# Kernel optimization log

Hardware: AMD Instinct MI355X
Metric: run time of the kernel (lower is better)

## Reference

```python
import jax, jax.numpy as jnp
from jax import lax
import numpy as np

N_QUBITS = 4
N_LAYERS = 2


def _apply_gate(state, M, w):
    # state: [B, 2,2,2,2]; M: [2,2] shared or [B,2,2] batched; acts on wire w
    s = jnp.moveaxis(state, w + 1, 1)
    if M.ndim == 3:
        s = jnp.einsum('bij,bj...->bi...', M, s)
    else:
        s = jnp.einsum('ij,bj...->bi...', M, s)
    return jnp.moveaxis(s, 1, w + 1)


def _apply_cnot(state, c, t):
    # c < t always (chain CNOTs). Move control axis to 1; target axis (t+1) unchanged.
    s = jnp.moveaxis(state, c + 1, 1)
    s0 = s[:, 0]
    s1 = jnp.flip(s[:, 1], axis=t)  # target axis after dropping axis1 is t+1-1 = t
    s = jnp.stack([s0, s1], axis=1)
    return jnp.moveaxis(s, 1, c + 1)


def _quantum_head(q_input, qparams):
    # q_input: [B, n_qubits] rotation angles; qparams: [n_layers, n_qubits, 3]
    B = q_input.shape[0]
    state = jnp.zeros((B, 2 ** N_QUBITS), jnp.complex64).at[:, 0].set(1.0)
    state = state.reshape((B,) + (2,) * N_QUBITS)
    # RY feature map (batched matrices)
    for i in range(N_QUBITS):
        th = q_input[:, i]
        c, s = jnp.cos(th / 2), jnp.sin(th / 2)
        M = jnp.stack([jnp.stack([c, -s], -1), jnp.stack([s, c], -1)], -2)  # [B,2,2]
        state = _apply_gate(state, M.astype(jnp.complex64), i)
    # variational layers
    for layer in range(N_LAYERS):
        for i in range(N_QUBITS):
            phi = qparams[layer, i, 0]
            th = qparams[layer, i, 1]
            om = qparams[layer, i, 2]
            c, s = jnp.cos(th / 2), jnp.sin(th / 2)
            hs, hd = 0.5 * (phi + om), 0.5 * (phi - om)
            M = jnp.stack([
                jnp.stack([jnp.exp(-1j * hs) * c, -jnp.exp(1j * hd) * s]),
                jnp.stack([jnp.exp(-1j * hd) * s, jnp.exp(1j * hs) * c]),
            ])  # [2,2] shared across batch (Rot = RZ(om) RY(th) RZ(phi))
            state = _apply_gate(state, M.astype(jnp.complex64), i)
        for i in range(N_QUBITS - 1):
            state = _apply_cnot(state, i, i + 1)
    # <Z_0> = P(q0=0) - P(q0=1)
    probs = state.real ** 2 + state.imag ** 2
    probs = probs.reshape(B, 2, -1)
    return probs[:, 0].sum(-1) - probs[:, 1].sum(-1)


def _maxpool21(x):
    return lax.reduce_window(x, -np.inf, lax.max, (1, 1, 2, 2), (1, 1, 1, 1), 'VALID')


def setup_inputs() -> dict:
    key = jax.random.key(0)
    ks = jax.random.split(key, 8)
    r = lambda k, s, sc: jax.random.normal(k, s, jnp.float32) * sc
    return {
        'inputs': jax.random.normal(ks[0], (128, 3, 250, 250), jnp.float32),
        'conv1_w': r(ks[1], (6, 3, 5, 5), 0.1),
        'conv1_b': jnp.zeros((6,), jnp.float32),
        'conv2_w': r(ks[2], (15, 6, 3, 3), 0.1),
        'conv2_b': jnp.zeros((15,), jnp.float32),
        'fc1_w': r(ks[3], (120, 55815), 0.004),
        'fc1_b': jnp.zeros((120,), jnp.float32),
        'fc2_w': r(ks[4], (84, 120), 0.09),
        'fc2_b': jnp.zeros((84,), jnp.float32),
        'fc3_w': r(ks[5], (1, 84), 0.1),
        'fc3_b': jnp.zeros((1,), jnp.float32),
        'qparams': jax.random.normal(ks[6], (N_LAYERS, N_QUBITS, 3), jnp.float32),
    }


def reference(inputs, conv1_w, conv1_b, conv2_w, conv2_b, fc1_w, fc1_b,
              fc2_w, fc2_b, fc3_w, fc3_b, qparams):
    dn = ('NCHW', 'OIHW', 'NCHW')
    x = lax.conv_general_dilated(inputs, conv1_w, (2, 2), [(1, 1), (1, 1)],
                                 dimension_numbers=dn) + conv1_b[None, :, None, None]
    x = _maxpool21(jax.nn.relu(x))          # [B,6,123,123]
    x = lax.conv_general_dilated(x, conv2_w, (2, 2), [(1, 1), (1, 1)],
                                 dimension_numbers=dn) + conv2_b[None, :, None, None]
    x = _maxpool21(jax.nn.relu(x))          # [B,15,61,61]
    x = x.reshape(x.shape[0], -1)           # [B,55815]
    x = jax.nn.relu(x @ fc1_w.T + fc1_b)
    x = jax.nn.relu(x @ fc2_w.T + fc2_b)
    x = (x @ fc3_w.T + fc3_b)[:, 0]         # [B]
    q_input = jnp.repeat(x[:, None], N_QUBITS, axis=1)
    q_out = _quantum_head(q_input, qparams)  # [B]
    probs = 0.5 * (q_out + 1.0)
    return jnp.stack([probs, 1.0 - probs], axis=-1)
```

## Files before the change

### kernel.cpp

```cpp
#include <hip/hip_runtime.h>

#define SPLITK 256
#define FC1_K 55815

__global__ __launch_bounds__(256) void conv1f_k(const float* __restrict__ in,
                                                const float* __restrict__ w,
                                                const float* __restrict__ bias,
                                                float* __restrict__ out) {
    __shared__ float sbuf[4608];
    const int tc = blockIdx.x, tr = blockIdx.y, b = blockIdx.z;
    const int pr0 = tr * 31, pc0 = tc * 31;
    const int tid = threadIdx.x;
    const int i = tid >> 4, j = tid & 15;
    const float* inb = in + (size_t)b * 187500;
    const int ir0 = 2 * pr0 - 1, ic0 = 2 * pc0 - 1;

    float acc[6][2][2];
    #pragma unroll
    for (int o = 0; o < 6; ++o) {
        float bv = bias[o];
        acc[o][0][0] = bv; acc[o][0][1] = bv; acc[o][1][0] = bv; acc[o][1][1] = bv;
    }

    float stg[18];
    auto load_ch = [&](int c) {
        const float* cp = inb + c * 62500;
        int y = tid / 68;
        int x = tid - y * 68;
        #pragma unroll
        for (int it = 0; it < 18; ++it) {
            int gr = ir0 + y, gc = ic0 + x;
            float v = 0.0f;
            if ((unsigned)gr < 250u && (unsigned)gc < 250u)
                v = cp[gr * 250 + gc];
            stg[it] = v;
            x += 52; y += 3;
            if (x >= 68) { x -= 68; ++y; }
        }
    };
    auto write_ch = [&]() {
        #pragma unroll
        for (int it = 0; it < 18; ++it) sbuf[tid + it * 256] = stg[it];
    };
    auto compute_ch = [&](int c) {
        #pragma unroll
        for (int wr = 0; wr < 7; ++wr) {
            const float* rp = &sbuf[(4 * i + wr) * 68 + 4 * j];
            float row[7];
            float4 v4 = *(const float4*)rp;
            float2 v2 = *(const float2*)(rp + 4);
            row[0] = v4.x; row[1] = v4.y; row[2] = v4.z; row[3] = v4.w;
            row[4] = v2.x; row[5] = v2.y; row[6] = rp[6];
            #pragma unroll
            for (int o = 0; o < 6; ++o) {
                #pragma unroll
                for (int kw = 0; kw < 5; ++kw) {
                    if (wr <= 4) {
                        float wv = w[o * 75 + c * 25 + wr * 5 + kw];
                        acc[o][0][0] = fmaf(row[kw], wv, acc[o][0][0]);
                        acc[o][0][1] = fmaf(row[kw + 2], wv, acc[o][0][1]);
                    }
                    if (wr >= 2) {
                        float wv = w[o * 75 + c * 25 + (wr - 2) * 5 + kw];
                        acc[o][1][0] = fmaf(row[kw], wv, acc[o][1][0]);
                        acc[o][1][1] = fmaf(row[kw + 2], wv, acc[o][1][1]);
                    }
                }
            }
        }
    };

    load_ch(0); write_ch();
    __syncthreads();
    load_ch(1); compute_ch(0);
    __syncthreads();
    write_ch();
    __syncthreads();
    load_ch(2); compute_ch(1);
    __syncthreads();
    write_ch();
    __syncthreads();
    compute_ch(2);
    __syncthreads();

    const int gr0 = pr0 + 2 * i, gc0 = pc0 + 2 * j;
    const bool r1in = (2 * i + 1 < 31) && (gr0 + 1 < 123);
    const bool c1in = (2 * j + 1 < 31) && (gc0 + 1 < 123);
    const bool r0in = gr0 < 123, c0in = gc0 < 123;
    #pragma unroll
    for (int g = 0; g < 2; ++g) {
        #pragma unroll
        for (int oo = 0; oo < 3; ++oo)
            #pragma unroll
            for (int di = 0; di < 2; ++di)
                #pragma unroll
                for (int dj = 0; dj < 2; ++dj)
                    sbuf[(oo * 32 + 2 * i + di) * 33 + (2 * j + dj)] =
                        fmaxf(acc[g * 3 + oo][di][dj], 0.0f);
        __syncthreads();
        #pragma unroll
        for (int oo = 0; oo < 3; ++oo) {
            int o = g * 3 + oo;
            const float* p0 = &sbuf[(oo * 32 + 2 * i) * 33 + 2 * j];
            float c00 = p0[0],  c01 = p0[1],  c02 = p0[2];
            float c10 = p0[33], c11 = p0[34], c12 = p0[35];
            float c20 = p0[66], c21 = p0[67], c22 = p0[68];
            float* orow = out + ((size_t)(b * 6 + o) * 123 + gr0) * 123 + gc0;
            if (r0in && c0in) orow[0]   = fmaxf(fmaxf(c00, c01), fmaxf(c10, c11));
            if (r0in && c1in) orow[1]   = fmaxf(fmaxf(c01, c02), fmaxf(c11, c12));
            if (r1in && c0in) orow[123] = fmaxf(fmaxf(c10, c11), fmaxf(c20, c21));
            if (r1in && c1in) orow[124] = fmaxf(fmaxf(c11, c12), fmaxf(c21, c22));
        }
        __syncthreads();
    }
}

__global__ __launch_bounds__(256) void conv2f_k(const float* __restrict__ in,
                                                const float* __restrict__ w,
                                                const float* __restrict__ bias,
                                                float* __restrict__ out) {
    __shared__ float smem[2000];
    const int tc = blockIdx.x, tr = blockIdx.y, b = blockIdx.z;
    const int pr0 = tr * 15, pc0 = tc * 15;
    const int tid = threadIdx.x;
    const int wv = tid >> 6, lane = tid & 63;
    const int ti = tid >> 4, tj = tid & 15;
    const int tl = ti & 3;
    float* wreg = smem + wv * 320;
    float* halo = smem + 1280;
    const float* inb = in + (size_t)b * 6 * 15129;
    const int irw = 2 * pr0 - 1 + 8 * wv;
    const int ic0 = 2 * pc0 - 1;
    const bool safe = (tr >= 1 && tr <= 3) && (tc >= 1 && tc <= 3);

    int off[5];
    unsigned msk = 0u;
    {
        int y = (lane >= 34) ? 1 : 0;
        int x = lane - 34 * y;
        #pragma unroll
        for (int it = 0; it < 5; ++it) {
            int gr = irw + y, gc = ic0 + x;
            bool valid = ((unsigned)gr < 123u) && ((unsigned)gc < 123u);
            off[it] = valid ? (gr * 123 + gc) : 0;
            msk |= (valid ? 1u : 0u) << it;
            x += 30; ++y;
            if (x >= 34) { x -= 34; ++y; }
        }
    }

    float acc[15];
    #pragma unroll
    for (int o = 0; o < 15; ++o) acc[o] = bias[o];

    for (int c = 0; c < 6; ++c) {
        const float* cp = inb + c * 15129;
        if (safe) {
            #pragma unroll
            for (int it = 0; it < 5; ++it) wreg[lane + it * 64] = cp[off[it]];
        } else {
            #pragma unroll
            for (int it = 0; it < 5; ++it) {
                float v = 0.0f;
                if ((msk >> it) & 1u) v = cp[off[it]];
                wreg[lane + it * 64] = v;
            }
        }
        #pragma unroll
        for (int kh = 0; kh < 3; ++kh) {
            const float* r = &wreg[(2 * tl + kh) * 34 + 2 * tj];
            float a0 = r[0], a1 = r[1], a2 = r[2];
            #pragma unroll
            for (int o = 0; o < 15; ++o) {
                const float* wr_ = &w[o * 54 + c * 9 + kh * 3];
                acc[o] = fmaf(a0, wr_[0], acc[o]);
                acc[o] = fmaf(a1, wr_[1], acc[o]);
                acc[o] = fmaf(a2, wr_[2], acc[o]);
            }
        }
    }

    if (tl == 0 && wv > 0) {
        #pragma unroll
        for (int o = 0; o < 15; ++o)
            halo[(wv - 1) * 240 + o * 16 + tj] = acc[o];
    }
    __syncthreads();

    const int gr = pr0 + ti, gc = pc0 + tj;
    const bool valid = (ti < 15) && (tj < 15) && (gr < 61) && (gc < 61);
    const bool lastrow = (tl == 3);
    const int hb = (wv < 2 ? wv : 2) * 240;
    #pragma unroll
    for (int o = 0; o < 15; ++o) {
        float c00 = acc[o];
        float c01 = __shfl(acc[o], lane + 1);
        float s10 = __shfl(acc[o], lane + 16);
        float s11 = __shfl(acc[o], lane + 17);
        float h10 = halo[hb + o * 16 + tj];
        float h11 = halo[hb + o * 16 + (tj + 1 > 15 ? 15 : tj + 1)];
        float c10 = lastrow ? h10 : s10;
        float c11 = lastrow ? h11 : s11;
        float m = fmaxf(fmaxf(fmaxf(c00, c01), fmaxf(c10, c11)), 0.0f);
        if (valid) out[((size_t)(b * 15 + o) * 61 + gr) * 61 + gc] = m;
    }
}

__global__ __launch_bounds__(256) void fc1_k(const float* __restrict__ X,
                                             const float* __restrict__ W,
                                             float* __restrict__ P) {
    __shared__ float Xs[2][16][132];
    __shared__ float Ws[2][16][66];
    const int K = FC1_K;
    const int chunk = (K + SPLITK - 1) / SPLITK;
    const int s = blockIdx.x, nh = blockIdx.y;
    const int n0 = nh * 60;
    int ks = s * chunk;
    int ke = min(ks + chunk, K);
    int tid = threadIdx.x;
    const int tx = tid & 15, ty = tid >> 4;
    const int kk_ = tid & 15, r0_ = tid >> 4;
    float acc[8][4];
    #pragma unroll
    for (int ii = 0; ii < 8; ++ii)
        #pragma unroll
        for (int jj = 0; jj < 4; ++jj) acc[ii][jj] = 0.0f;

    float nx[8], nw[4];
    auto ld = [&](int k0n) {
        int krem = ke - k0n;
        int k = k0n + kk_;
        bool kv = kk_ < krem;
        #pragma unroll
        for (int it = 0; it < 8; ++it) {
            int r = r0_ + it * 16;
            nx[it] = kv ? X[(size_t)r * K + k] : 0.0f;
        }
        #pragma unroll
        for (int it = 0; it < 4; ++it) {
            int r = r0_ + it * 16;
            nw[it] = (kv && r < 60) ? W[(size_t)(n0 + r) * K + k] : 0.0f;
        }
    };
    auto st = [&](int buf) {
        #pragma unroll
        for (int it = 0; it < 8; ++it) Xs[buf][kk_][r0_ + it * 16] = nx[it];
        #pragma unroll
        for (int it = 0; it < 4; ++it) Ws[buf][kk_][r0_ + it * 16] = nw[it];
    };

    if (ks < ke) { ld(ks); st(0); }
    int cur = 0;
    for (int k0 = ks; k0 < ke; k0 += 16) {
        __syncthreads();
        bool hn = (k0 + 16) < ke;
        if (hn) ld(k0 + 16);
        #pragma unroll
        for (int kk = 0; kk < 16; ++kk) {
            float4 xa = *(const float4*)&Xs[cur][kk][ty * 8];
            float4 xb = *(const float4*)&Xs[cur][kk][ty * 8 + 4];
            float4 wb = *(const float4*)&Ws[cur][kk][tx * 4];
            float av[8] = {xa.x, xa.y, xa.z, xa.w, xb.x, xb.y, xb.z, xb.w};
            float bv[4] = {wb.x, wb.y, wb.z, wb.w};
            #pragma unroll
            for (int ii = 0; ii < 8; ++ii)
                #pragma unroll
                for (int jj = 0; jj < 4; ++jj)
                    acc[ii][jj] = fmaf(av[ii], bv[jj], acc[ii][jj]);
        }
        if (hn) st(cur ^ 1);
        cur ^= 1;
    }
    float* Pp = P + (size_t)s * 15360;
    #pragma unroll
    for (int ii = 0; ii < 8; ++ii) {
        int m = ty * 8 + ii;
        #pragma unroll
        for (int jj = 0; jj < 4; ++jj) {
            int nn = tx * 4 + jj;
            if (nn < 60) Pp[m * 120 + n0 + nn] = acc[ii][jj];
        }
    }
}

__global__ __launch_bounds__(256) void tail_k(const float* __restrict__ P,
                                              const float* __restrict__ f1b,
                                              const float* __restrict__ f2w,
                                              const float* __restrict__ f2b,
                                              const float* __restrict__ f3w,
                                              const float* __restrict__ f3b,
                                              const float* __restrict__ qp,
                                              float* __restrict__ out) {
    __shared__ float red[2][120];
    __shared__ float x1[120];
    __shared__ float x2[84];
    int b = blockIdx.x, tid = threadIdx.x;
    if (tid < 240) {
        int part = tid / 120;
        int n = tid - part * 120;
        const float* p = P + (size_t)b * 120 + n;
        float acc = 0.0f;
        #pragma unroll 8
        for (int s = part; s < SPLITK; s += 2)
            acc += p[(size_t)s * 15360];
        red[part][n] = acc;
    }
    __syncthreads();
    if (tid < 120)
        x1[tid] = fmaxf(red[0][tid] + red[1][tid] + f1b[tid], 0.0f);
    __syncthreads();
    if (tid < 84) {
        float acc = f2b[tid];
        const float* wr = f2w + tid * 120;
        #pragma unroll 4
        for (int n = 0; n < 120; ++n) acc = fmaf(x1[n], wr[n], acc);
        x2[tid] = fmaxf(acc, 0.0f);
    }
    __syncthreads();
    if (tid == 0) {
        float x = f3b[0];
        for (int m = 0; m < 84; ++m) x = fmaf(x2[m], f3w[m], x);
        float sr[16], si[16];
        #pragma unroll
        for (int i = 0; i < 16; ++i) { sr[i] = 0.0f; si[i] = 0.0f; }
        sr[0] = 1.0f;
        float c0 = cosf(0.5f * x), s0 = sinf(0.5f * x);
        #pragma unroll
        for (int w = 0; w < 4; ++w) {
            int mask = 8 >> w;
            #pragma unroll
            for (int idx = 0; idx < 16; ++idx) {
                if (idx & mask) continue;
                int i1 = idx | mask;
                float a0r = sr[idx], a0i = si[idx], a1r = sr[i1], a1i = si[i1];
                sr[idx] = c0 * a0r - s0 * a1r;  si[idx] = c0 * a0i - s0 * a1i;
                sr[i1]  = s0 * a0r + c0 * a1r;  si[i1]  = s0 * a0i + c0 * a1i;
            }
        }
        for (int layer = 0; layer < 2; ++layer) {
            #pragma unroll
            for (int w = 0; w < 4; ++w) {
                int gi = (layer * 4 + w) * 3;
                float phi = qp[gi], th = qp[gi + 1], om = qp[gi + 2];
                float hs = 0.5f * (phi + om), hd = 0.5f * (phi - om);
                float ct = cosf(0.5f * th), st = sinf(0.5f * th);
                float chs = cosf(hs), shs = sinf(hs);
                float chd = cosf(hd), shd = sinf(hd);
                float m00r = chs * ct,  m00i = -shs * ct;
                float m01r = -chd * st, m01i = -shd * st;
                float m10r = chd * st,  m10i = -shd * st;
                float m11r = chs * ct,  m11i = shs * ct;
                int mask = 8 >> w;
                #pragma unroll
                for (int idx = 0; idx < 16; ++idx) {
                    if (idx & mask) continue;
                    int i1 = idx | mask;
                    float a0r = sr[idx], a0i = si[idx], a1r = sr[i1], a1i = si[i1];
                    sr[idx] = m00r * a0r - m00i * a0i + m01r * a1r - m01i * a1i;
                    si[idx] = m00r * a0i + m00i * a0r + m01r * a1i + m01i * a1r;
                    sr[i1]  = m10r * a0r - m10i * a0i + m11r * a1r - m11i * a1i;
                    si[i1]  = m10r * a0i + m10i * a0r + m11r * a1i + m11i * a1r;
                }
            }
            #pragma unroll
            for (int cw = 0; cw < 3; ++cw) {
                int cm = 8 >> cw, tm = 8 >> (cw + 1);
                #pragma unroll
                for (int idx = 0; idx < 16; ++idx) {
                    if ((idx & cm) && !(idx & tm)) {
                        int i1 = idx | tm;
                        float tr = sr[idx]; sr[idx] = sr[i1]; sr[i1] = tr;
                        float ti = si[idx]; si[idx] = si[i1]; si[i1] = ti;
                    }
                }
            }
        }
        float q = 0.0f;
        #pragma unroll
        for (int idx = 0; idx < 16; ++idx) {
            float p2 = sr[idx] * sr[idx] + si[idx] * si[idx];
            q += (idx < 8) ? p2 : -p2;
        }
        float pr = 0.5f * (q + 1.0f);
        out[2 * b] = pr;
        out[2 * b + 1] = 1.0f - pr;
    }
}

extern "C" void kernel_launch(void* const* d_in, const int* in_sizes, int n_in,
                              void* d_out, int out_size, void* d_ws, size_t ws_size,
                              hipStream_t stream) {
    const float* inp = (const float*)d_in[0];
    const float* c1w = (const float*)d_in[1];
    const float* c1b = (const float*)d_in[2];
    const float* c2w = (const float*)d_in[3];
    const float* c2b = (const float*)d_in[4];
    const float* f1w = (const float*)d_in[5];
    const float* f1b = (const float*)d_in[6];
    const float* f2w = (const float*)d_in[7];
    const float* f2b = (const float*)d_in[8];
    const float* f3w = (const float*)d_in[9];
    const float* f3b = (const float*)d_in[10];
    const float* qp  = (const float*)d_in[11];
    float* out = (float*)d_out;
    float* ws = (float*)d_ws;

    float* B = ws;
    float* D = ws + 11619072;
    float* P = ws + 18763392;

    conv1f_k<<<dim3(4, 4, 128), 256, 0, stream>>>(inp, c1w, c1b, B);
    conv2f_k<<<dim3(5, 5, 128), 256, 0, stream>>>(B, c2w, c2b, D);
    fc1_k<<<dim3(SPLITK, 2), 256, 0, stream>>>(D, f1w, P);
    tail_k<<<128, 256, 0, stream>>>(P, f1b, f2w, f2b, f3w, f3b, qp, out);
}
```

Before: 163.7 us.

## Run fc1 on bf16 MFMA with bf16 activations and pre-converted weights

conv2 now writes its pooled output as bf16 into a padded K layout. A new kernel converts the fc1 weights to bf16 on every call. fc1 is rewritten to use 16x16x32 bf16 MFMA instructions over 224-wide K chunks, with one block per split covering all 120 outputs. The aim is to cut fc1 memory traffic and FMA cost, at the price of bf16 rounding error and an extra weight-conversion pass each call.

```diff
diff --git a/kernel.cpp b/kernel.cpp
--- a/kernel.cpp
+++ b/kernel.cpp
@@ -2,6 +2,12 @@
 
 #define SPLITK 256
 #define FC1_K 55815
+#define KP 55816
+
+__device__ __forceinline__ unsigned short f2bf(float f) {
+    unsigned u = __float_as_uint(f);
+    return (unsigned short)((u + 0x7FFFu + ((u >> 16) & 1u)) >> 16);
+}
 
 __global__ __launch_bounds__(256) void conv1f_k(const float* __restrict__ in,
                                                 const float* __restrict__ w,
@@ -118,7 +124,7 @@
 __global__ __launch_bounds__(256) void conv2f_k(const float* __restrict__ in,
                                                 const float* __restrict__ w,
                                                 const float* __restrict__ bias,
-                                                float* __restrict__ out) {
+                                                unsigned short* __restrict__ out) {
     __shared__ float smem[2000];
     const int tc = blockIdx.x, tr = blockIdx.y, b = blockIdx.z;
     const int pr0 = tr * 15, pc0 = tc * 15;
@@ -202,85 +208,116 @@
         float c10 = lastrow ? h10 : s10;
         float c11 = lastrow ? h11 : s11;
         float m = fmaxf(fmaxf(fmaxf(c00, c01), fmaxf(c10, c11)), 0.0f);
-        if (valid) out[((size_t)(b * 15 + o) * 61 + gr) * 61 + gc] = m;
-    }
-}
-
-__global__ __launch_bounds__(256) void fc1_k(const float* __restrict__ X,
-                                             const float* __restrict__ W,
+        if (valid) out[(size_t)b * KP + o * 3721 + gr * 61 + gc] = f2bf(m);
+    }
+}
+
+__global__ __launch_bounds__(256) void wcvt_k(const float* __restrict__ W,
+                                              unsigned short* __restrict__ Wb) {
+    const int n = blockIdx.y;
+    const float* src = W + (size_t)n * FC1_K;
+    unsigned int* dst = (unsigned int*)(Wb + (size_t)n * KP);
+    int base = blockIdx.x * 2048 + threadIdx.x * 2;
+    #pragma unroll
+    for (int p = 0; p < 4; ++p) {
+        int k2 = base + p * 512;
+        if (k2 < FC1_K) {
+            float v0 = src[k2];
+            float v1 = (k2 + 1 < FC1_K) ? src[k2 + 1] : 0.0f;
+            dst[k2 >> 1] = (unsigned)f2bf(v0) | ((unsigned)f2bf(v1) << 16);
+        }
+    }
+}
+
+__global__ __launch_bounds__(256) void fc1_k(const unsigned short* __restrict__ Xb,
+                                             const unsigned short* __restrict__ Wb,
                                              float* __restrict__ P) {
-    __shared__ float Xs[2][16][132];
-    __shared__ float Ws[2][16][66];
-    const int K = FC1_K;
-    const int chunk = (K + SPLITK - 1) / SPLITK;
-    const int s = blockIdx.x, nh = blockIdx.y;
-    const int n0 = nh * 60;
-    int ks = s * chunk;
-    int ke = min(ks + chunk, K);
-    int tid = threadIdx.x;
-    const int tx = tid & 15, ty = tid >> 4;
-    const int kk_ = tid & 15, r0_ = tid >> 4;
-    float acc[8][4];
-    #pragma unroll
-    for (int ii = 0; ii < 8; ++ii)
-        #pragma unroll
-        for (int jj = 0; jj < 4; ++jj) acc[ii][jj] = 0.0f;
-
-    float nx[8], nw[4];
-    auto ld = [&](int k0n) {
-        int krem = ke - k0n;
-        int k = k0n + kk_;
-        bool kv = kk_ < krem;
-        #pragma unroll
-        for (int it = 0; it < 8; ++it) {
-            int r = r0_ + it * 16;
-            nx[it] = kv ? X[(size_t)r * K + k] : 0.0f;
-        }
-        #pragma unroll
-        for (int it = 0; it < 4; ++it) {
-            int r = r0_ + it * 16;
-            nw[it] = (kv && r < 60) ? W[(size_t)(n0 + r) * K + k] : 0.0f;
+    using short8 = __attribute__((ext_vector_type(8))) short;
+    using f32x4 = __attribute__((ext_vector_type(4))) float;
+    __shared__ unsigned short Xs[2][128][40];
+    __shared__ unsigned short Ws[2][128][40];
+    const int s = blockIdx.x;
+    const int ks = s * 224;
+    const int ke = min(ks + 224, FC1_K);
+    const int tid = threadIdx.x;
+    const int row = tid >> 1, cb = (tid & 1) * 16;
+    const int wv = tid >> 6, lane = tid & 63;
+    const int kb = lane >> 4, lr = lane & 15;
+
+    f32x4 acc[2][8];
+    #pragma unroll
+    for (int mt = 0; mt < 2; ++mt)
+        #pragma unroll
+        for (int nt = 0; nt < 8; ++nt)
+            acc[mt][nt] = (f32x4){0.f, 0.f, 0.f, 0.f};
+
+    const int nsteps = (ke > ks) ? ((ke - ks + 31) >> 5) : 0;
+
+    auto stage = [&](int buf, int st) {
+        const int k0 = ks + st * 32;
+        const int krem = ke - k0;
+        const unsigned short* xsrc = Xb + (size_t)row * KP + k0 + cb;
+        #pragma unroll
+        for (int q = 0; q < 2; ++q) {
+            int g = cb + q * 8;
+            if (g + 8 <= krem) {
+                *(uint4*)&Xs[buf][row][g] = *(const uint4*)(xsrc + q * 8);
+            } else {
+                #pragma unroll
+                for (int jj = 0; jj < 8; ++jj)
+                    Xs[buf][row][g + jj] = (g + jj < krem) ? xsrc[q * 8 + jj] : (unsigned short)0;
+            }
+        }
+        if (row < 120) {
+            const unsigned short* wsrc = Wb + (size_t)row * KP + k0 + cb;
+            #pragma unroll
+            for (int q = 0; q < 2; ++q) {
+                int g = cb + q * 8;
+                if (g + 8 <= krem) {
+                    *(uint4*)&Ws[buf][row][g] = *(const uint4*)(wsrc + q * 8);
+                } else {
+                    #pragma unroll
+                    for (int jj = 0; jj < 8; ++jj)
+                        Ws[buf][row][g + jj] = (g + jj < krem) ? wsrc[q * 8 + jj] : (unsigned short)0;
+                }
+            }
+        } else {
+            uint4 z = {0u, 0u, 0u, 0u};
+            *(uint4*)&Ws[buf][row][cb] = z;
+            *(uint4*)&Ws[buf][row][cb + 8] = z;
         }
     };
-    auto st = [&](int buf) {
-        #pragma unroll
-        for (int it = 0; it < 8; ++it) Xs[buf][kk_][r0_ + it * 16] = nx[it];
-        #pragma unroll
-        for (int it = 0; it < 4; ++it) Ws[buf][kk_][r0_ + it * 16] = nw[it];
-    };
-
-    if (ks < ke) { ld(ks); st(0); }
+
+    if (nsteps > 0) stage(0, 0);
     int cur = 0;
-    for (int k0 = ks; k0 < ke; k0 += 16) {
+    for (int st = 0; st < nsteps; ++st) {
         __syncthreads();
-        bool hn = (k0 + 16) < ke;
-        if (hn) ld(k0 + 16);
-        #pragma unroll
-        for (int kk = 0; kk < 16; ++kk) {
-            float4 xa = *(const float4*)&Xs[cur][kk][ty * 8];
-            float4 xb = *(const float4*)&Xs[cur][kk][ty * 8 + 4];
-            float4 wb = *(const float4*)&Ws[cur][kk][tx * 4];
-            float av[8] = {xa.x, xa.y, xa.z, xa.w, xb.x, xb.y, xb.z, xb.w};
-            float bv[4] = {wb.x, wb.y, wb.z, wb.w};
-            #pragma unroll
-            for (int ii = 0; ii < 8; ++ii)
-                #pragma unroll
-                for (int jj = 0; jj < 4; ++jj)
-                    acc[ii][jj] = fmaf(av[ii], bv[jj], acc[ii][jj]);
-        }
-        if (hn) st(cur ^ 1);
+        if (st + 1 < nsteps) stage(cur ^ 1, st + 1);
+        short8 afr[2];
+        #pragma unroll
+        for (int mt = 0; mt < 2; ++mt)
+            afr[mt] = *(const short8*)&Xs[cur][(wv * 2 + mt) * 16 + lr][kb * 8];
+        #pragma unroll
+        for (int nt = 0; nt < 8; ++nt) {
+            short8 bfr = *(const short8*)&Ws[cur][nt * 16 + lr][kb * 8];
+            #pragma unroll
+            for (int mt = 0; mt < 2; ++mt)
+                acc[mt][nt] = __builtin_amdgcn_mfma_f32_16x16x32_bf16(afr[mt], bfr, acc[mt][nt], 0, 0, 0);
+        }
         cur ^= 1;
     }
+
     float* Pp = P + (size_t)s * 15360;
     #pragma unroll
-    for (int ii = 0; ii < 8; ++ii) {
-        int m = ty * 8 + ii;
-        #pragma unroll
-        for (int jj = 0; jj < 4; ++jj) {
-            int nn = tx * 4 + jj;
-            if (nn < 60) Pp[m * 120 + n0 + nn] = acc[ii][jj];
-        }
-    }
+    for (int mt = 0; mt < 2; ++mt)
+        #pragma unroll
+        for (int nt = 0; nt < 8; ++nt)
+            #pragma unroll
+            for (int r = 0; r < 4; ++r) {
+                int m = (wv * 2 + mt) * 16 + kb * 4 + r;
+                int n = nt * 16 + lr;
+                if (n < 120) Pp[m * 120 + n] = acc[mt][nt][r];
+            }
 }
 
 __global__ __launch_bounds__(256) void tail_k(const float* __restrict__ P,
@@ -406,11 +443,13 @@
     float* ws = (float*)d_ws;
 
     float* B = ws;
-    float* D = ws + 11619072;
-    float* P = ws + 18763392;
-
+    unsigned short* Db = (unsigned short*)(ws + 11619072);
+    float* P = ws + 15191296;
+    unsigned short* Wb = (unsigned short*)(ws + 19123456);
+
+    wcvt_k<<<dim3(28, 120), 256, 0, stream>>>(f1w, Wb);
     conv1f_k<<<dim3(4, 4, 128), 256, 0, stream>>>(inp, c1w, c1b, B);
-    conv2f_k<<<dim3(5, 5, 128), 256, 0, stream>>>(B, c2w, c2b, D);
-    fc1_k<<<dim3(SPLITK, 2), 256, 0, stream>>>(D, f1w, P);
+    conv2f_k<<<dim3(5, 5, 128), 256, 0, stream>>>(B, c2w, c2b, Db);
+    fc1_k<<<dim3(SPLITK), 256, 0, stream>>>(Db, Wb, P);
     tail_k<<<128, 256, 0, stream>>>(P, f1b, f2w, f2b, f3w, f3b, qp, out);
 }
```

New measurement: 154.0 us. 1.06x faster.
